# Kernel tuning notes

Hardware: AMD Instinct MI355X
Metric: run time of the kernel (lower is better)

## Reference

```python
import jax, jax.numpy as jnp
import numpy as np

N = 100000
DEG = 16
E = N * DEG
IN_F = 128
OUT_F = 64
ALPHA = 0.2  # LeakyReLU negative slope


def setup_inputs() -> dict:
    key = jax.random.key(0)
    k1, k2, k3, k4, k5, k6 = jax.random.split(key, 6)
    x = jax.random.normal(k1, (N, IN_F), dtype=jnp.float32)
    # src = repeat(arange(N), DEG) guarantees every node has outgoing edges
    # (original torch code divides by the out-edge score sum -> NaN otherwise).
    src = jnp.repeat(jnp.arange(N, dtype=jnp.int64), DEG)
    dst = jax.random.randint(k2, (E,), 0, N, dtype=jnp.int64)
    edges = jnp.stack([src, dst], axis=0)
    # Conv1d(in, out, k=1, bias=False) == linear with weight [out, in]
    w_seq = jax.random.normal(k3, (OUT_F, IN_F), dtype=jnp.float32) / np.sqrt(IN_F)
    # a_1, a_2: Conv1d(out, 1, k=1) with bias
    a1_w = jax.random.normal(k4, (OUT_F,), dtype=jnp.float32) / np.sqrt(OUT_F)
    a1_b = jnp.zeros((), dtype=jnp.float32)
    a2_w = jax.random.normal(k5, (OUT_F,), dtype=jnp.float32) / np.sqrt(OUT_F)
    a2_b = jnp.zeros((), dtype=jnp.float32)
    bias = jnp.zeros((OUT_F,), dtype=jnp.float32)
    return {"x": x, "edges": edges, "w_seq": w_seq, "a1_w": a1_w,
            "a1_b": a1_b, "a2_w": a2_w, "a2_b": a2_b, "bias": bias}


def reference(x, edges, w_seq, a1_w, a1_b, a2_w, a2_b, bias):
    src, dst = edges[0], edges[1]
    feat = x @ w_seq.T                       # [N, OUT_F]
    a1 = feat @ a1_w + a1_b                  # [N]
    a2 = feat @ a2_w + a2_b                  # [N]
    score = a1[src] + a2[dst]                # [E]
    score = jnp.exp(jax.nn.leaky_relu(score, ALPHA))
    score_sum = jax.ops.segment_sum(score, src, num_segments=N)  # [N]
    # sparse COO (score at (src,dst)) @ feat == segment_sum of score * feat[dst]
    msgs = score[:, None] * feat[dst]        # [E, OUT_F]
    agg = jax.ops.segment_sum(msgs, src, num_segments=N)         # [N, OUT_F]
    out = agg / score_sum[:, None] + bias
    return out
```

## Files before the change

kernel.cpp:

```cpp
#include <hip/hip_runtime.h>
#include <stdint.h>

#define N_NODES 100000
#define DEG 16
#define IN_F 128
#define OUT_F 64
#define ALPHA 0.2f

typedef __attribute__((ext_vector_type(8))) short short8;
typedef __attribute__((ext_vector_type(4))) float f32x4;
typedef __attribute__((ext_vector_type(4))) int i32x4;
typedef __attribute__((ext_vector_type(2))) unsigned int u32x2;

static __device__ __forceinline__ unsigned short f2bf(float f) {
    uint32_t u = __float_as_uint(f);
    u += 0x7FFFu + ((u >> 16) & 1u);
    return (unsigned short)(u >> 16);
}

__global__ __launch_bounds__(256) void prep_kernel(
    const float* __restrict__ w, const float* __restrict__ a1w,
    const float* __restrict__ a2w, unsigned short* __restrict__ wb,
    float* __restrict__ v1, float* __restrict__ v2)
{
    int idx = blockIdx.x * 256 + threadIdx.x;
    if (idx < OUT_F * IN_F) wb[idx] = f2bf(w[idx]);
    if (blockIdx.x == 0) {
        int t = threadIdx.x;
        int k = t & (IN_F - 1);
        const float* aw = (t < IN_F) ? a1w : a2w;
        float acc = 0.f;
        #pragma unroll
        for (int f = 0; f < OUT_F; ++f) acc += w[f * IN_F + k] * aw[f];
        if (t < IN_F) v1[k] = acc; else v2[k] = acc;
    }
}

__global__ __launch_bounds__(256) void gat_feat_kernel(
    const float* __restrict__ x, const unsigned short* __restrict__ wb,
    const float* __restrict__ v1, const float* __restrict__ v2,
    const float* __restrict__ a1bp, const float* __restrict__ a2bp,
    unsigned short* __restrict__ featb, float* __restrict__ a1,
    float* __restrict__ a2)
{
    __shared__ __align__(16) unsigned short lds[4][32][64];
    const int wid  = threadIdx.x >> 6;
    const int lane = threadIdx.x & 63;
    const int r = lane & 15;
    const int g = lane >> 4;
    const int base = (blockIdx.x * 4 + wid) * 32;
    if (base >= N_NODES) return;

    f32x4 acc[2][4];
    #pragma unroll
    for (int mt = 0; mt < 2; ++mt)
        #pragma unroll
        for (int ft = 0; ft < 4; ++ft) acc[mt][ft] = (f32x4){0.f, 0.f, 0.f, 0.f};
    float p1[2] = {0.f, 0.f}, p2[2] = {0.f, 0.f};

    #pragma unroll
    for (int ks = 0; ks < 4; ++ks) {
        short8 bf[4];
        #pragma unroll
        for (int ft = 0; ft < 4; ++ft)
            bf[ft] = *(const short8*)(wb + (ft * 16 + r) * IN_F + ks * 32 + g * 8);
        const float* vp1 = v1 + ks * 32 + g * 8;
        const float* vp2 = v2 + ks * 32 + g * 8;
        f32x4 v10 = *(const f32x4*)(vp1),     v11 = *(const f32x4*)(vp1 + 4);
        f32x4 v20 = *(const f32x4*)(vp2),     v21 = *(const f32x4*)(vp2 + 4);
        #pragma unroll
        for (int mt = 0; mt < 2; ++mt) {
            const float* xp = x + (size_t)(base + mt * 16 + r) * IN_F + ks * 32 + g * 8;
            f32x4 x0 = *(const f32x4*)(xp);
            f32x4 x1 = *(const f32x4*)(xp + 4);
            #pragma unroll
            for (int j = 0; j < 4; ++j) {
                p1[mt] += x0[j] * v10[j] + x1[j] * v11[j];
                p2[mt] += x0[j] * v20[j] + x1[j] * v21[j];
            }
            short8 af;
            af[0] = (short)f2bf(x0[0]); af[1] = (short)f2bf(x0[1]);
            af[2] = (short)f2bf(x0[2]); af[3] = (short)f2bf(x0[3]);
            af[4] = (short)f2bf(x1[0]); af[5] = (short)f2bf(x1[1]);
            af[6] = (short)f2bf(x1[2]); af[7] = (short)f2bf(x1[3]);
            #pragma unroll
            for (int ft = 0; ft < 4; ++ft)
                acc[mt][ft] = __builtin_amdgcn_mfma_f32_16x16x32_bf16(af, bf[ft], acc[mt][ft], 0, 0, 0);
        }
    }

    #pragma unroll
    for (int mt = 0; mt < 2; ++mt) {
        p1[mt] += __shfl_xor(p1[mt], 16, 64);
        p1[mt] += __shfl_xor(p1[mt], 32, 64);
        p2[mt] += __shfl_xor(p2[mt], 16, 64);
        p2[mt] += __shfl_xor(p2[mt], 32, 64);
    }
    if (lane < 16) {
        float b1 = a1bp[0], b2 = a2bp[0];
        #pragma unroll
        for (int mt = 0; mt < 2; ++mt) {
            a1[base + mt * 16 + lane] = p1[mt] + b1;
            a2[base + mt * 16 + lane] = p2[mt] + b2;
        }
    }

    #pragma unroll
    for (int mt = 0; mt < 2; ++mt)
        #pragma unroll
        for (int ft = 0; ft < 4; ++ft)
            #pragma unroll
            for (int reg = 0; reg < 4; ++reg)
                lds[wid][mt * 16 + g * 4 + reg][ft * 16 + r] = f2bf(acc[mt][ft][reg]);
    const char* lsrc = (const char*)(&lds[wid][0][0]);
    char* gdst = (char*)featb + (size_t)base * (OUT_F * 2);
    #pragma unroll
    for (int t = 0; t < 4; ++t) {
        i32x4 v = *(const i32x4*)(lsrc + t * 1024 + lane * 16);
        *(i32x4*)(gdst + t * 1024 + lane * 16) = v;
    }
}

__global__ __launch_bounds__(256) void gat_agg_kernel(
    const int* __restrict__ dst, const unsigned short* __restrict__ featb,
    const float* __restrict__ a1, const float* __restrict__ a2,
    const float* __restrict__ bias, float* __restrict__ out)
{
    const int wid  = threadIdx.x >> 6;
    const int lane = threadIdx.x & 63;
    const int q  = lane >> 4;
    const int e0 = lane & 15;
    const int i = (blockIdx.x * 4 + wid) * 4 + q;
    const int sb = lane & 48;

    const int d = dst[i * DEG + e0];
    const float z = a1[i] + a2[d];
    const float s = __expf(fmaxf(z, ALPHA * z));

    float se[16];
    float acc0 = 0.f, acc1 = 0.f, acc2 = 0.f, acc3 = 0.f;

    int de[8];
    #pragma unroll
    for (int e = 0; e < 8; ++e) de[e] = __shfl(d, sb + e, 64);
    u32x2 u[8];
    #pragma unroll
    for (int e = 0; e < 8; ++e)
        u[e] = *(const u32x2*)(featb + ((size_t)de[e] * OUT_F + e0 * 4));
    #pragma unroll
    for (int e = 0; e < 16; ++e) se[e] = __shfl(s, sb + e, 64);
    float ssum = 0.f;
    #pragma unroll
    for (int e = 0; e < 16; ++e) ssum += se[e];
    #pragma unroll
    for (int e = 0; e < 8; ++e) {
        acc0 += se[e] * __uint_as_float(u[e][0] << 16);
        acc1 += se[e] * __uint_as_float(u[e][0] & 0xffff0000u);
        acc2 += se[e] * __uint_as_float(u[e][1] << 16);
        acc3 += se[e] * __uint_as_float(u[e][1] & 0xffff0000u);
    }

    #pragma unroll
    for (int e = 0; e < 8; ++e) de[e] = __shfl(d, sb + 8 + e, 64);
    #pragma unroll
    for (int e = 0; e < 8; ++e)
        u[e] = *(const u32x2*)(featb + ((size_t)de[e] * OUT_F + e0 * 4));
    #pragma unroll
    for (int e = 0; e < 8; ++e) {
        acc0 += se[8 + e] * __uint_as_float(u[e][0] << 16);
        acc1 += se[8 + e] * __uint_as_float(u[e][0] & 0xffff0000u);
        acc2 += se[8 + e] * __uint_as_float(u[e][1] << 16);
        acc3 += se[8 + e] * __uint_as_float(u[e][1] & 0xffff0000u);
    }

    const float inv = 1.0f / ssum;
    const f32x4 bv = *(const f32x4*)(bias + e0 * 4);
    f32x4 o;
    o[0] = acc0 * inv + bv[0];
    o[1] = acc1 * inv + bv[1];
    o[2] = acc2 * inv + bv[2];
    o[3] = acc3 * inv + bv[3];
    *(f32x4*)(out + (size_t)i * OUT_F + e0 * 4) = o;
}

extern "C" void kernel_launch(void* const* d_in, const int* in_sizes, int n_in,
                              void* d_out, int out_size, void* d_ws, size_t ws_size,
                              hipStream_t stream) {
    (void)in_sizes; (void)n_in; (void)out_size; (void)ws_size;
    const float* x    = (const float*)d_in[0];
    const int*   edges= (const int*)d_in[1];
    const float* w    = (const float*)d_in[2];
    const float* a1w  = (const float*)d_in[3];
    const float* a1b  = (const float*)d_in[4];
    const float* a2w  = (const float*)d_in[5];
    const float* a2b  = (const float*)d_in[6];
    const float* bias = (const float*)d_in[7];
    float* out = (float*)d_out;

    unsigned short* featb = (unsigned short*)d_ws;
    float* a1 = (float*)((char*)d_ws + (size_t)N_NODES * OUT_F * 2);
    float* a2 = a1 + N_NODES;
    float* v1 = a2 + N_NODES;
    float* v2 = v1 + IN_F;
    unsigned short* wb = (unsigned short*)(v2 + IN_F);

    const int* dst = edges + (size_t)N_NODES * DEG;

    prep_kernel<<<dim3((OUT_F * IN_F + 255) / 256), dim3(256), 0, stream>>>(
        w, a1w, a2w, wb, v1, v2);
    gat_feat_kernel<<<dim3((N_NODES + 127) / 128), dim3(256), 0, stream>>>(
        x, wb, v1, v2, a1b, a2b, featb, a1, a2);
    gat_agg_kernel<<<dim3((N_NODES + 15) / 16), dim3(256), 0, stream>>>(
        dst, featb, a1, a2, bias, out);
}
```

Measured before the change: 57.83 us.

## Restructure feat and agg kernels: prefetch x, swizzle LDS, 16-byte gathers

The feature kernel now runs one wave per block and issues every x load up front as non-temporal loads. It swaps the hand-written bf16 rounding for the packed hardware conversion and XOR-swizzles the LDS staging buffer to cut bank conflicts. The aggregation kernel gathers 16-byte feature chunks, with each lane pair splitting the edges and combining partial sums by shuffle. It also reduces the score sum with a butterfly instead of 16 broadcasts and issues the gathers before the exp. The aim is fewer, wider memory requests and more loads in flight, at the cost of more registers and extra shuffles.

```diff
diff --git a/kernel.cpp b/kernel.cpp
--- a/kernel.cpp
+++ b/kernel.cpp
@@ -1,4 +1,5 @@
 #include <hip/hip_runtime.h>
+#include <hip/hip_bf16.h>
 #include <stdint.h>
 
 #define N_NODES 100000
@@ -10,12 +11,15 @@
 typedef __attribute__((ext_vector_type(8))) short short8;
 typedef __attribute__((ext_vector_type(4))) float f32x4;
 typedef __attribute__((ext_vector_type(4))) int i32x4;
-typedef __attribute__((ext_vector_type(2))) unsigned int u32x2;
-
+typedef __attribute__((ext_vector_type(4))) unsigned int u32x4;
+
+static __device__ __forceinline__ unsigned int pack2bf(float lo, float hi) {
+    __hip_bfloat162 h = __float22bfloat162_rn(make_float2(lo, hi));
+    unsigned int u; __builtin_memcpy(&u, &h, 4); return u;
+}
 static __device__ __forceinline__ unsigned short f2bf(float f) {
-    uint32_t u = __float_as_uint(f);
-    u += 0x7FFFu + ((u >> 16) & 1u);
-    return (unsigned short)(u >> 16);
+    __hip_bfloat16 h = __float2bfloat16(f);
+    unsigned short u; __builtin_memcpy(&u, &h, 2); return u;
 }
 
 __global__ __launch_bounds__(256) void prep_kernel(
@@ -36,20 +40,29 @@
     }
 }
 
-__global__ __launch_bounds__(256) void gat_feat_kernel(
+__global__ __launch_bounds__(64) void gat_feat_kernel(
     const float* __restrict__ x, const unsigned short* __restrict__ wb,
     const float* __restrict__ v1, const float* __restrict__ v2,
     const float* __restrict__ a1bp, const float* __restrict__ a2bp,
     unsigned short* __restrict__ featb, float* __restrict__ a1,
     float* __restrict__ a2)
 {
-    __shared__ __align__(16) unsigned short lds[4][32][64];
-    const int wid  = threadIdx.x >> 6;
+    __shared__ __align__(16) unsigned short lds[32][64];
     const int lane = threadIdx.x & 63;
     const int r = lane & 15;
     const int g = lane >> 4;
-    const int base = (blockIdx.x * 4 + wid) * 32;
-    if (base >= N_NODES) return;
+    const unsigned base = blockIdx.x * 32;
+
+    f32x4 xr[2][4][2];
+    #pragma unroll
+    for (int mt = 0; mt < 2; ++mt) {
+        const float* xrow = x + (size_t)(base + mt * 16 + r) * IN_F + g * 8;
+        #pragma unroll
+        for (int ks = 0; ks < 4; ++ks) {
+            xr[mt][ks][0] = __builtin_nontemporal_load((const f32x4*)(xrow + ks * 32));
+            xr[mt][ks][1] = __builtin_nontemporal_load((const f32x4*)(xrow + ks * 32 + 4));
+        }
+    }
 
     f32x4 acc[2][4];
     #pragma unroll
@@ -66,23 +79,22 @@
             bf[ft] = *(const short8*)(wb + (ft * 16 + r) * IN_F + ks * 32 + g * 8);
         const float* vp1 = v1 + ks * 32 + g * 8;
         const float* vp2 = v2 + ks * 32 + g * 8;
-        f32x4 v10 = *(const f32x4*)(vp1),     v11 = *(const f32x4*)(vp1 + 4);
-        f32x4 v20 = *(const f32x4*)(vp2),     v21 = *(const f32x4*)(vp2 + 4);
+        f32x4 v10 = *(const f32x4*)(vp1), v11 = *(const f32x4*)(vp1 + 4);
+        f32x4 v20 = *(const f32x4*)(vp2), v21 = *(const f32x4*)(vp2 + 4);
         #pragma unroll
         for (int mt = 0; mt < 2; ++mt) {
-            const float* xp = x + (size_t)(base + mt * 16 + r) * IN_F + ks * 32 + g * 8;
-            f32x4 x0 = *(const f32x4*)(xp);
-            f32x4 x1 = *(const f32x4*)(xp + 4);
+            f32x4 x0 = xr[mt][ks][0], x1 = xr[mt][ks][1];
             #pragma unroll
             for (int j = 0; j < 4; ++j) {
                 p1[mt] += x0[j] * v10[j] + x1[j] * v11[j];
                 p2[mt] += x0[j] * v20[j] + x1[j] * v21[j];
             }
-            short8 af;
-            af[0] = (short)f2bf(x0[0]); af[1] = (short)f2bf(x0[1]);
-            af[2] = (short)f2bf(x0[2]); af[3] = (short)f2bf(x0[3]);
-            af[4] = (short)f2bf(x1[0]); af[5] = (short)f2bf(x1[1]);
-            af[6] = (short)f2bf(x1[2]); af[7] = (short)f2bf(x1[3]);
+            u32x4 au;
+            au[0] = pack2bf(x0[0], x0[1]);
+            au[1] = pack2bf(x0[2], x0[3]);
+            au[2] = pack2bf(x1[0], x1[1]);
+            au[3] = pack2bf(x1[2], x1[3]);
+            short8 af; __builtin_memcpy(&af, &au, 16);
             #pragma unroll
             for (int ft = 0; ft < 4; ++ft)
                 acc[mt][ft] = __builtin_amdgcn_mfma_f32_16x16x32_bf16(af, bf[ft], acc[mt][ft], 0, 0, 0);
@@ -108,16 +120,20 @@
     #pragma unroll
     for (int mt = 0; mt < 2; ++mt)
         #pragma unroll
-        for (int ft = 0; ft < 4; ++ft)
+        for (int ft = 0; ft < 4; ++ft) {
+            const int cp = (ft * 16 + r) ^ (g << 4);
             #pragma unroll
             for (int reg = 0; reg < 4; ++reg)
-                lds[wid][mt * 16 + g * 4 + reg][ft * 16 + r] = f2bf(acc[mt][ft][reg]);
-    const char* lsrc = (const char*)(&lds[wid][0][0]);
+                lds[mt * 16 + g * 4 + reg][cp] = f2bf(acc[mt][ft][reg]);
+        }
     char* gdst = (char*)featb + (size_t)base * (OUT_F * 2);
     #pragma unroll
     for (int t = 0; t < 4; ++t) {
-        i32x4 v = *(const i32x4*)(lsrc + t * 1024 + lane * 16);
-        *(i32x4*)(gdst + t * 1024 + lane * 16) = v;
+        const int row = t * 8 + (lane >> 3);
+        const int cl  = (lane & 7) * 8;
+        const int cp  = cl ^ (((row >> 2) & 3) << 4);
+        i32x4 v = *(const i32x4*)(&lds[row][cp]);
+        *(i32x4*)(gdst + (size_t)row * 128 + cl * 2) = v;
     }
 }
 
@@ -128,59 +144,50 @@
 {
     const int wid  = threadIdx.x >> 6;
     const int lane = threadIdx.x & 63;
-    const int q  = lane >> 4;
     const int e0 = lane & 15;
-    const int i = (blockIdx.x * 4 + wid) * 4 + q;
+    const int eh = (lane >> 3) & 1;
+    const int fq = lane & 7;
     const int sb = lane & 48;
-
-    const int d = dst[i * DEG + e0];
+    const int i = (blockIdx.x * 4 + wid) * 4 + (lane >> 4);
+
+    const int d = __builtin_nontemporal_load(dst + i * DEG + e0);
+
+    u32x4 u[8];
+    #pragma unroll
+    for (int t = 0; t < 8; ++t) {
+        const int de = __shfl(d, sb + 2 * t + eh, 64);
+        u[t] = *(const u32x4*)(featb + (unsigned)de * OUT_F + fq * 8);
+    }
+
     const float z = a1[i] + a2[d];
     const float s = __expf(fmaxf(z, ALPHA * z));
-
-    float se[16];
-    float acc0 = 0.f, acc1 = 0.f, acc2 = 0.f, acc3 = 0.f;
-
-    int de[8];
-    #pragma unroll
-    for (int e = 0; e < 8; ++e) de[e] = __shfl(d, sb + e, 64);
-    u32x2 u[8];
-    #pragma unroll
-    for (int e = 0; e < 8; ++e)
-        u[e] = *(const u32x2*)(featb + ((size_t)de[e] * OUT_F + e0 * 4));
-    #pragma unroll
-    for (int e = 0; e < 16; ++e) se[e] = __shfl(s, sb + e, 64);
-    float ssum = 0.f;
-    #pragma unroll
-    for (int e = 0; e < 16; ++e) ssum += se[e];
-    #pragma unroll
-    for (int e = 0; e < 8; ++e) {
-        acc0 += se[e] * __uint_as_float(u[e][0] << 16);
-        acc1 += se[e] * __uint_as_float(u[e][0] & 0xffff0000u);
-        acc2 += se[e] * __uint_as_float(u[e][1] << 16);
-        acc3 += se[e] * __uint_as_float(u[e][1] & 0xffff0000u);
-    }
-
-    #pragma unroll
-    for (int e = 0; e < 8; ++e) de[e] = __shfl(d, sb + 8 + e, 64);
-    #pragma unroll
-    for (int e = 0; e < 8; ++e)
-        u[e] = *(const u32x2*)(featb + ((size_t)de[e] * OUT_F + e0 * 4));
-    #pragma unroll
-    for (int e = 0; e < 8; ++e) {
-        acc0 += se[8 + e] * __uint_as_float(u[e][0] << 16);
-        acc1 += se[8 + e] * __uint_as_float(u[e][0] & 0xffff0000u);
-        acc2 += se[8 + e] * __uint_as_float(u[e][1] << 16);
-        acc3 += se[8 + e] * __uint_as_float(u[e][1] & 0xffff0000u);
-    }
+    float ssum = s;
+    #pragma unroll
+    for (int m = 1; m <= 8; m <<= 1) ssum += __shfl_xor(ssum, m, 64);
+    float se[8];
+    #pragma unroll
+    for (int t = 0; t < 8; ++t) se[t] = __shfl(s, sb + 2 * t + eh, 64);
+
+    float acc[8] = {0.f,0.f,0.f,0.f,0.f,0.f,0.f,0.f};
+    #pragma unroll
+    for (int t = 0; t < 8; ++t)
+        #pragma unroll
+        for (int w = 0; w < 4; ++w) {
+            acc[2 * w]     += se[t] * __uint_as_float(u[t][w] << 16);
+            acc[2 * w + 1] += se[t] * __uint_as_float(u[t][w] & 0xffff0000u);
+        }
+    #pragma unroll
+    for (int j = 0; j < 8; ++j) acc[j] += __shfl_xor(acc[j], 8, 64);
 
     const float inv = 1.0f / ssum;
-    const f32x4 bv = *(const f32x4*)(bias + e0 * 4);
+    const f32x4 bv = *(const f32x4*)(bias + fq * 8 + eh * 4);
     f32x4 o;
-    o[0] = acc0 * inv + bv[0];
-    o[1] = acc1 * inv + bv[1];
-    o[2] = acc2 * inv + bv[2];
-    o[3] = acc3 * inv + bv[3];
-    *(f32x4*)(out + (size_t)i * OUT_F + e0 * 4) = o;
+    #pragma unroll
+    for (int j = 0; j < 4; ++j) {
+        const float aj = eh ? acc[4 + j] : acc[j];
+        o[j] = aj * inv + bv[j];
+    }
+    __builtin_nontemporal_store(o, (f32x4*)(out + (unsigned)i * OUT_F + fq * 8 + eh * 4));
 }
 
 extern "C" void kernel_launch(void* const* d_in, const int* in_sizes, int n_in,
@@ -208,8 +215,8 @@
 
     prep_kernel<<<dim3((OUT_F * IN_F + 255) / 256), dim3(256), 0, stream>>>(
         w, a1w, a2w, wb, v1, v2);
-    gat_feat_kernel<<<dim3((N_NODES + 127) / 128), dim3(256), 0, stream>>>(
+    gat_feat_kernel<<<dim3(N_NODES / 32), dim3(64), 0, stream>>>(
         x, wb, v1, v2, a1b, a2b, featb, a1, a2);
-    gat_agg_kernel<<<dim3((N_NODES + 15) / 16), dim3(256), 0, stream>>>(
+    gat_agg_kernel<<<dim3(N_NODES / 16), dim3(256), 0, stream>>>(
         dst, featb, a1, a2, bias, out);
 }
```

After: 80.64 us. 39.5% more time.
